# Performance work log

Hardware: AMD Instinct MI355X
Metric: run time of the kernel (lower is better)

## Reference

```python
import jax, jax.numpy as jnp
import numpy as np
import math

TOP_K = 2
CAP_FACTOR = 1.25
AUX_W = 0.01


def setup_inputs() -> dict:
    key = jax.random.key(0)
    k1, k2 = jax.random.split(key)
    x = jax.random.normal(k1, (8192, 4096), dtype=jnp.float32)
    # gate weight, torch init std=0.01, stored as (E, D) like nn.Linear
    gate_w = jax.random.normal(k2, (64, 4096), dtype=jnp.float32) * 0.01
    return {"x": x, "gate_w": gate_w}


def reference(x, gate_w):
    N, D = x.shape
    E = gate_w.shape[0]
    K = TOP_K
    C = max(math.ceil(CAP_FACTOR * N / E), 1)  # expert capacity

    logits = x @ gate_w.T                      # (N, E)
    probs = jax.nn.softmax(logits, axis=-1)    # (N, E)
    vals, idx = jax.lax.top_k(probs, K)        # (N, K)
    vals = vals / vals.sum(axis=-1, keepdims=True)

    # Parallel replacement of the serial double loop: flatten (N,K) row-major
    # (token-major, then k) which matches the loop iteration order exactly.
    flat_e = idx.reshape(-1)                               # (N*K,) expert ids
    oh = jax.nn.one_hot(flat_e, E, dtype=jnp.int32)        # (N*K, E)
    # exclusive prefix count of prior assignments to each expert
    pos = jnp.cumsum(oh, axis=0) - oh                      # (N*K, E)
    slot = jnp.take_along_axis(pos, flat_e[:, None], axis=1)[:, 0]  # (N*K,)
    # In the torch loop the counter saturates at C (only incremented when
    # c < C), so slot==prior_total is equivalent: kept iff prior_total < C.
    keep = slot < C
    slot_s = jnp.where(keep, slot, 0)
    tok = jnp.arange(N * K) // K

    combine_weights = jnp.zeros((N, E, C), dtype=x.dtype).at[
        tok, flat_e, slot_s].add(jnp.where(keep, vals.reshape(-1), 0.0))
    dispatch_mask = (jnp.zeros((N, E, C), dtype=jnp.int32).at[
        tok, flat_e, slot_s].add(keep.astype(jnp.int32))) > 0

    # load balancing loss
    f = oh.astype(jnp.float32).reshape(N, K, E).mean(axis=(0, 1))  # (E,)
    p = probs.mean(axis=0)                                         # (E,)
    load_loss = AUX_W * E * jnp.sum(f * p)

    return dispatch_mask, combine_weights, probs, load_loss
```

## Files before the change

kernel.cpp:

```cpp
#include <hip/hip_runtime.h>
#include <math.h>

#define N_TOK 8192
#define DIM   4096
#define NEXP  64
#define CAP   160
#define OFF_CW    (83886080ULL)
#define OFF_PROBS (167772160ULL)
#define OFF_LOSS  (168296448ULL)
#define NA    16384
#define SPLIT 8

__device__ __forceinline__ float wave_max64(float v) {
    for (int m = 1; m < 64; m <<= 1) v = fmaxf(v, __shfl_xor(v, m, 64));
    return v;
}
__device__ __forceinline__ float wave_sum64(float v) {
    for (int m = 1; m < 64; m <<= 1) v += __shfl_xor(v, m, 64);
    return v;
}
__device__ __forceinline__ void wave_argmax64(float& v, int& i) {
    for (int m = 1; m < 64; m <<= 1) {
        float ov = __shfl_xor(v, m, 64);
        int   oi = __shfl_xor(i, m, 64);
        if (ov > v || (ov == v && oi < i)) { v = ov; i = oi; }
    }
}

__global__ __launch_bounds__(256) void k_gemm(const float* __restrict__ x,
                                              const float* __restrict__ gw,
                                              float* __restrict__ part) {
    __shared__ float xs[64][68];
    __shared__ float wsh[64][68];
    const int tb = (blockIdx.x & 127) * 64;
    const int sy = blockIdx.x >> 7;
    const int d_begin = sy * (DIM / SPLIT);
    const int t  = threadIdx.x;
    const int tx = t & 15, ty = t >> 4;
    float acc[4][4] = {};
    for (int ci = 0; ci < (DIM / SPLIT) / 64; ++ci) {
        const int d0 = d_begin + ci * 64;
        for (int it = 0; it < 4; ++it) {
            int idx = t + 256 * it;
            int row = idx >> 4;
            int d4  = idx & 15;
            *(float4*)(&xs[row][4 * d4]) =
                *(const float4*)(x + (size_t)(tb + row) * DIM + d0 + 4 * d4);
            *(float4*)(&wsh[row][4 * d4]) =
                *(const float4*)(gw + (size_t)row * DIM + d0 + 4 * d4);
        }
        __syncthreads();
        for (int d4 = 0; d4 < 16; ++d4) {
            float4 xa[4], wb[4];
            for (int i = 0; i < 4; ++i) xa[i] = *(const float4*)(&xs[ty + 16 * i][4 * d4]);
            for (int j = 0; j < 4; ++j) wb[j] = *(const float4*)(&wsh[tx + 16 * j][4 * d4]);
            for (int i = 0; i < 4; ++i)
                for (int j = 0; j < 4; ++j) {
                    acc[i][j] = fmaf(xa[i].x, wb[j].x, acc[i][j]);
                    acc[i][j] = fmaf(xa[i].y, wb[j].y, acc[i][j]);
                    acc[i][j] = fmaf(xa[i].z, wb[j].z, acc[i][j]);
                    acc[i][j] = fmaf(xa[i].w, wb[j].w, acc[i][j]);
                }
        }
        __syncthreads();
    }
    for (int i = 0; i < 4; ++i)
        for (int j = 0; j < 4; ++j)
            part[(size_t)sy * N_TOK * NEXP +
                 (size_t)(tb + ty + 16 * i) * NEXP + (tx + 16 * j)] = acc[i][j];
}

__global__ __launch_bounds__(256) void k_router(const float* __restrict__ part,
                                                float* __restrict__ probs_out,
                                                int* __restrict__ rec_e,
                                                float* __restrict__ rec_w) {
    const int tok  = blockIdx.x * 4 + (threadIdx.x >> 6);
    const int lane = threadIdx.x & 63;
    float l = 0.f;
    for (int s = 0; s < SPLIT; ++s)
        l += part[(size_t)s * N_TOK * NEXP + (size_t)tok * NEXP + lane];
    const float m  = wave_max64(l);
    const float ex = expf(l - m);
    const float sm = wave_sum64(ex);
    const float p  = ex / sm;
    probs_out[(size_t)tok * NEXP + lane] = p;
    float v1 = p; int i1 = lane;
    wave_argmax64(v1, i1);
    float v2 = (lane == i1) ? -1.f : p; int i2 = lane;
    wave_argmax64(v2, i2);
    if (lane == 0) {
        const float denom = v1 + v2;
        rec_e[2 * tok]     = i1;
        rec_e[2 * tok + 1] = i2;
        rec_w[2 * tok]     = v1 / denom;
        rec_w[2 * tok + 1] = v2 / denom;
    }
}

__global__ __launch_bounds__(256) void k_preduce(const float* __restrict__ probs,
                                                 float* __restrict__ psum_part) {
    __shared__ float sh[256];
    const int e = threadIdx.x & 63, tg = threadIdx.x >> 6;
    const int tok0 = blockIdx.x * 128;
    float a = 0.f;
    for (int k = 0; k < 32; ++k)
        a += probs[(size_t)(tok0 + tg + 4 * k) * NEXP + e];
    sh[threadIdx.x] = a;
    __syncthreads();
    if (threadIdx.x < 64)
        psum_part[blockIdx.x * 64 + threadIdx.x] =
            sh[threadIdx.x] + sh[64 + threadIdx.x] +
            sh[128 + threadIdx.x] + sh[192 + threadIdx.x];
}

__global__ __launch_bounds__(256) void k_assign_scatter(const int* __restrict__ rec_e,
                                                        const float* __restrict__ rec_w,
                                                        const float* __restrict__ psum_part,
                                                        float* __restrict__ out) {
    if (blockIdx.x == 16) {
        __shared__ int hcnt[64];
        if (threadIdx.x < 64) hcnt[threadIdx.x] = 0;
        __syncthreads();
        for (int j = 0; j < 64; ++j) {
            const int e = rec_e[j * 256 + threadIdx.x];
            atomicAdd(&hcnt[e], 1);
        }
        __syncthreads();
        if (threadIdx.x < 64) {
            const int e = threadIdx.x;
            float ps = 0.f;
            for (int b = 0; b < 64; ++b) ps += psum_part[b * 64 + e];
            float term = ((float)hcnt[e] / (float)NA) * (ps / (float)N_TOK);
            term = wave_sum64(term);
            if (e == 0) out[OFF_LOSS] = 0.01f * 64.f * term;
        }
        return;
    }
    const int w    = blockIdx.x * 4 + (threadIdx.x >> 6);
    const int lane = threadIdx.x & 63;
    int base = 0;
    const unsigned long long ltmask = (1ull << lane) - 1ull;
    #pragma unroll 4
    for (int c = 0; c < NA / 64; ++c) {
        const int i = c * 64 + lane;
        const int e = rec_e[i];
        const unsigned long long mask = __ballot(e == w);
        if (e == w) {
            const int slot = base + __popcll(mask & ltmask);
            if (slot < CAP) {
                const int tok = i >> 1;
                const size_t off = (size_t)tok * (NEXP * CAP) + (size_t)w * CAP + slot;
                out[off]          = 1.0f;
                out[OFF_CW + off] = rec_w[i];
            }
        }
        base += __popcll(mask);
    }
}

extern "C" void kernel_launch(void* const* d_in, const int* in_sizes, int n_in,
                              void* d_out, int out_size, void* d_ws, size_t ws_size,
                              hipStream_t stream) {
    const float* x  = (const float*)d_in[0];
    const float* gw = (const float*)d_in[1];
    float* out = (float*)d_out;

    char* w = (char*)d_ws;
    float* part      = (float*)w;
    int*   rec_e     = (int*)(w + (size_t)SPLIT * N_TOK * NEXP * 4);
    float* rec_w     = (float*)((char*)rec_e + NA * 4);
    float* psum_part = (float*)((char*)rec_w + NA * 4);

    k_gemm<<<1024, 256, 0, stream>>>(x, gw, part);
    k_router<<<2048, 256, 0, stream>>>(part, out + OFF_PROBS, rec_e, rec_w);
    k_preduce<<<64, 256, 0, stream>>>(out + OFF_PROBS, psum_part);
    k_assign_scatter<<<17, 256, 0, stream>>>(rec_e, rec_w, psum_part, out);
}
```

Baseline: 746.3 us.

## Replace FP32 SIMT gate GEMM with split-bf16 MFMA (3-term) GEMM

Converts the router GEMM from scalar FP32 FMAs through LDS tiles to bf16 MFMA 16x16x32 instructions. It keeps near-FP32 accuracy by splitting each operand into high and low bf16 parts and summing three products. Gate weights are pre-split by a new small kernel. Activations are split in registers and read directly from global memory without LDS staging. The aim is to raise matrix throughput, at the cost of 3x the MFMA work and some loss of precision versus true FP32.

```diff
diff --git a/kernel.cpp b/kernel.cpp
--- a/kernel.cpp
+++ b/kernel.cpp
@@ -10,6 +10,29 @@
 #define OFF_LOSS  (168296448ULL)
 #define NA    16384
 #define SPLIT 8
+#define KSL   (DIM / SPLIT)
+#define CHUNKS (KSL / 32)
+
+typedef short  bf16x8 __attribute__((ext_vector_type(8)));
+typedef float  f32x4  __attribute__((ext_vector_type(4)));
+
+__device__ __forceinline__ unsigned short f2bf(float f) {
+    unsigned int u = __float_as_uint(f);
+    return (unsigned short)((u + 0x7FFFu + ((u >> 16) & 1u)) >> 16);
+}
+__device__ __forceinline__ float bf2f(unsigned short h) {
+    return __uint_as_float(((unsigned int)h) << 16);
+}
+__device__ __forceinline__ void split8(const float4 a0, const float4 a1,
+                                       bf16x8& h, bf16x8& l) {
+    const float v[8] = {a0.x, a0.y, a0.z, a0.w, a1.x, a1.y, a1.z, a1.w};
+    #pragma unroll
+    for (int e = 0; e < 8; ++e) {
+        const unsigned short hh = f2bf(v[e]);
+        h[e] = (short)hh;
+        l[e] = (short)f2bf(v[e] - bf2f(hh));
+    }
+}
 
 __device__ __forceinline__ float wave_max64(float v) {
     for (int m = 1; m < 64; m <<= 1) v = fmaxf(v, __shfl_xor(v, m, 64));
@@ -27,47 +50,78 @@
     }
 }
 
-__global__ __launch_bounds__(256) void k_gemm(const float* __restrict__ x,
-                                              const float* __restrict__ gw,
-                                              float* __restrict__ part) {
-    __shared__ float xs[64][68];
-    __shared__ float wsh[64][68];
-    const int tb = (blockIdx.x & 127) * 64;
-    const int sy = blockIdx.x >> 7;
-    const int d_begin = sy * (DIM / SPLIT);
-    const int t  = threadIdx.x;
-    const int tx = t & 15, ty = t >> 4;
-    float acc[4][4] = {};
-    for (int ci = 0; ci < (DIM / SPLIT) / 64; ++ci) {
-        const int d0 = d_begin + ci * 64;
-        for (int it = 0; it < 4; ++it) {
-            int idx = t + 256 * it;
-            int row = idx >> 4;
-            int d4  = idx & 15;
-            *(float4*)(&xs[row][4 * d4]) =
-                *(const float4*)(x + (size_t)(tb + row) * DIM + d0 + 4 * d4);
-            *(float4*)(&wsh[row][4 * d4]) =
-                *(const float4*)(gw + (size_t)row * DIM + d0 + 4 * d4);
-        }
-        __syncthreads();
-        for (int d4 = 0; d4 < 16; ++d4) {
-            float4 xa[4], wb[4];
-            for (int i = 0; i < 4; ++i) xa[i] = *(const float4*)(&xs[ty + 16 * i][4 * d4]);
-            for (int j = 0; j < 4; ++j) wb[j] = *(const float4*)(&wsh[tx + 16 * j][4 * d4]);
-            for (int i = 0; i < 4; ++i)
-                for (int j = 0; j < 4; ++j) {
-                    acc[i][j] = fmaf(xa[i].x, wb[j].x, acc[i][j]);
-                    acc[i][j] = fmaf(xa[i].y, wb[j].y, acc[i][j]);
-                    acc[i][j] = fmaf(xa[i].z, wb[j].z, acc[i][j]);
-                    acc[i][j] = fmaf(xa[i].w, wb[j].w, acc[i][j]);
-                }
-        }
-        __syncthreads();
-    }
+__global__ __launch_bounds__(256) void k_wsplit(const float* __restrict__ gw,
+                                                unsigned short* __restrict__ wh,
+                                                unsigned short* __restrict__ wl) {
+    const float* src = gw + (size_t)blockIdx.x * DIM;
+    unsigned short* dh = wh + (size_t)blockIdx.x * DIM;
+    unsigned short* dl = wl + (size_t)blockIdx.x * DIM;
+    for (int i = threadIdx.x; i < DIM / 4; i += 256) {
+        const float4 v = *(const float4*)(src + 4 * i);
+        ushort4 h, l;
+        h.x = f2bf(v.x); l.x = f2bf(v.x - bf2f(h.x));
+        h.y = f2bf(v.y); l.y = f2bf(v.y - bf2f(h.y));
+        h.z = f2bf(v.z); l.z = f2bf(v.z - bf2f(h.z));
+        h.w = f2bf(v.w); l.w = f2bf(v.w - bf2f(h.w));
+        *(ushort4*)(dh + 4 * i) = h;
+        *(ushort4*)(dl + 4 * i) = l;
+    }
+}
+
+__global__ __launch_bounds__(256) void k_gemm_mfma(const float* __restrict__ x,
+                                                   const unsigned short* __restrict__ wh,
+                                                   const unsigned short* __restrict__ wl,
+                                                   float* __restrict__ part) {
+    const int sy   = blockIdx.x >> 5;
+    const int tb   = (blockIdx.x & 31) * 256;
+    const int wv   = (threadIdx.x >> 6);
+    const int lane = threadIdx.x & 63;
+    const int r16  = lane & 15;
+    const int kro  = (lane >> 4) * 8;
+    const int tokb = tb + wv * 64;
+
+    f32x4 acc[4][4];
+    #pragma unroll
     for (int i = 0; i < 4; ++i)
-        for (int j = 0; j < 4; ++j)
-            part[(size_t)sy * N_TOK * NEXP +
-                 (size_t)(tb + ty + 16 * i) * NEXP + (tx + 16 * j)] = acc[i][j];
+        #pragma unroll
+        for (int j = 0; j < 4; ++j) acc[i][j] = (f32x4){0.f, 0.f, 0.f, 0.f};
+
+    for (int c = 0; c < CHUNKS; ++c) {
+        const size_t k0 = (size_t)sy * KSL + c * 32 + kro;
+        bf16x8 bhf[4], blf[4];
+        #pragma unroll
+        for (int j = 0; j < 4; ++j) {
+            const size_t wo = (size_t)(j * 16 + r16) * DIM + k0;
+            bhf[j] = *(const bf16x8*)(wh + wo);
+            blf[j] = *(const bf16x8*)(wl + wo);
+        }
+        #pragma unroll
+        for (int i = 0; i < 4; ++i) {
+            const float* ap = x + (size_t)(tokb + i * 16 + r16) * DIM + k0;
+            const float4 a0 = *(const float4*)(ap);
+            const float4 a1 = *(const float4*)(ap + 4);
+            bf16x8 ah, al;
+            split8(a0, a1, ah, al);
+            #pragma unroll
+            for (int j = 0; j < 4; ++j) {
+                acc[i][j] = __builtin_amdgcn_mfma_f32_16x16x32_bf16(ah, bhf[j], acc[i][j], 0, 0, 0);
+                acc[i][j] = __builtin_amdgcn_mfma_f32_16x16x32_bf16(al, bhf[j], acc[i][j], 0, 0, 0);
+                acc[i][j] = __builtin_amdgcn_mfma_f32_16x16x32_bf16(ah, blf[j], acc[i][j], 0, 0, 0);
+            }
+        }
+    }
+    float* pb = part + (size_t)sy * N_TOK * NEXP;
+    #pragma unroll
+    for (int i = 0; i < 4; ++i) {
+        const int trow = tokb + i * 16 + (lane >> 4) * 4;
+        #pragma unroll
+        for (int j = 0; j < 4; ++j) {
+            const int e = j * 16 + r16;
+            #pragma unroll
+            for (int r = 0; r < 4; ++r)
+                pb[(size_t)(trow + r) * NEXP + e] = acc[i][j][r];
+        }
+    }
 }
 
 __global__ __launch_bounds__(256) void k_router(const float* __restrict__ part,
@@ -170,8 +224,11 @@
     int*   rec_e     = (int*)(w + (size_t)SPLIT * N_TOK * NEXP * 4);
     float* rec_w     = (float*)((char*)rec_e + NA * 4);
     float* psum_part = (float*)((char*)rec_w + NA * 4);
-
-    k_gemm<<<1024, 256, 0, stream>>>(x, gw, part);
+    unsigned short* wh = (unsigned short*)((char*)psum_part + 64 * 64 * 4);
+    unsigned short* wl = wh + (size_t)NEXP * DIM;
+
+    k_wsplit<<<64, 256, 0, stream>>>(gw, wh, wl);
+    k_gemm_mfma<<<256, 256, 0, stream>>>(x, wh, wl, part);
     k_router<<<2048, 256, 0, stream>>>(part, out + OFF_PROBS, rec_e, rec_w);
     k_preduce<<<64, 256, 0, stream>>>(out + OFF_PROBS, psum_part);
     k_assign_scatter<<<17, 256, 0, stream>>>(rec_e, rec_w, psum_part, out);
```

Measured after the change: 722.4 us. -3.2%, faster.
